# Kernel optimization log

Measured on AMD Instinct MI355X. Metric: run time of the kernel, lower is better.

## Reference

```python
import jax, jax.numpy as jnp
import numpy as np

NU, NI = 50000, 50000
N = NU + NI
NNZ = 1_000_000
DIM = 64          # dim_latent
FK = 4            # factor_k
DK = DIM // FK    # dim_k = 16
ITER_K = 2        # iterate_k
NUM_LAYER = 2     # len(dim_layer_list)
EPS = 1e-12


def setup_inputs() -> dict:
    key = jax.random.key(0)
    k1, k2, k3, k4 = jax.random.split(key, 4)
    # xavier-ish init scale for the embedding tables
    embed_user = jax.random.normal(k1, (NU, DIM), dtype=jnp.float32) * 0.1
    embed_item = jax.random.normal(k2, (NI, DIM), dtype=jnp.float32) * 0.1
    edge_head = jax.random.randint(k3, (NNZ,), 0, N, dtype=jnp.int32)
    edge_tail = jax.random.randint(k4, (NNZ,), 0, N, dtype=jnp.int32)
    return {"embed_user": embed_user, "embed_item": embed_item,
            "edge_head": edge_head, "edge_tail": edge_tail}


def _l2norm(x, axis=-1):
    # torch F.normalize(p=2): x / max(||x||, eps)
    return x / jnp.maximum(jnp.linalg.norm(x, axis=axis, keepdims=True), EPS)


def _dgcf_forward(embed_user, embed_item, head, tail):
    ego = jnp.concatenate([embed_user, embed_item], axis=0)  # [N, DIM]
    A_values = jnp.ones((FK, NNZ), dtype=ego.dtype)
    all_embed = [ego]

    def spmm(v, x):
        # sparse A (values v on edges head->tail) @ x : [N, DK]
        return jax.ops.segment_sum(v[:, None] * x[tail], head, num_segments=N)

    spmm_f = jax.vmap(spmm)  # over factor axis

    for _ in range(NUM_LAYER):
        # split ego into factor chunks: [FK, N, DK]
        xs = jnp.moveaxis(ego.reshape(N, FK, DK), 1, 0)
        factor_emb = None
        for t in range(ITER_K):
            # softmax over factors per edge; detached (as in torch .detach())
            vals = jax.lax.stop_gradient(jax.nn.softmax(A_values, axis=0))  # [FK, NNZ]
            # row sums of each factor adjacency -> D = diag(1/sqrt(rowsum))
            row_sum = jax.ops.segment_sum(vals.T, head, num_segments=N).T   # [FK, N]
            d = jnp.where(row_sum > 0,
                          1.0 / jnp.sqrt(jnp.maximum(row_sum, EPS)), 0.0)
            # factor_emb = D @ A @ D @ x  (three chained spmm in torch)
            y = spmm_f(vals, d[:, :, None] * xs)
            factor_emb = d[:, :, None] * y                                   # [FK, N, DK]
            # routing scores: sum over dim of normalize(h) * tanh(normalize(t))
            h = _l2norm(factor_emb[:, head, :], -1)                          # [FK, NNZ, DK]
            tt = _l2norm(xs[:, tail, :], -1)
            scores = jnp.sum(h * jnp.tanh(tt), axis=-1)                      # [FK, NNZ]
            A_values = A_values + scores
        # layer output: normalize last-iteration factor embeddings, re-concat
        layer_emb = _l2norm(factor_emb, -1)           # [FK, N, DK]
        ego = jnp.moveaxis(layer_emb, 0, 1).reshape(N, DIM)
        all_embed.append(ego)

    out = jnp.mean(jnp.stack(all_embed, axis=1), axis=1)  # [N, DIM]
    return out


def reference(embed_user, embed_item, edge_head, edge_tail):
    out = _dgcf_forward(embed_user, embed_item, edge_head, edge_tail)
    return out[:NU], out[NU:]
```

## Files before the change

kernel.cpp:

```cpp
#include <hip/hip_runtime.h>
#include <hip/hip_bf16.h>

#define NUSER 50000
#define NITEM 50000
#define NN    100000
#define NNZ_  1000000
#define DIM_  64
#define NBLK  391
#define EPB   2560
#define BINC  4096
#define NPAD  (NBLK * BINC)

#define FL_SVC    1
#define FL_SC     2
#define FL_NEXT   8
#define FL_FIN    16
#define FL_ACONST 32
#define FL_GN     128

static inline int ceil_div(int a, int b) { return (a + b - 1) / b; }

static __device__ inline float bf2f(unsigned short u) {
    return __uint_as_float(((unsigned int)u) << 16);
}
static __device__ inline unsigned short f2bf(float f) {
    unsigned int x = __float_as_uint(f);
    x += 0x7fffu + ((x >> 16) & 1u);
    return (unsigned short)(x >> 16);
}
static __device__ inline unsigned short f2h(float f) {
    _Float16 h = (_Float16)f;
    return __builtin_bit_cast(unsigned short, h);
}
static __device__ inline float h2f(unsigned short u) {
    return (float)__builtin_bit_cast(_Float16, u);
}

#if __has_builtin(__builtin_amdgcn_fdot2_f32_bf16)
typedef __bf16 bf16x2_t __attribute__((ext_vector_type(2)));
static __device__ inline float dot2bf(unsigned int a, unsigned int b, float c) {
    return __builtin_amdgcn_fdot2_f32_bf16(__builtin_bit_cast(bf16x2_t, a),
                                           __builtin_bit_cast(bf16x2_t, b), c, false);
}
#else
static __device__ inline float dot2bf(unsigned int a, unsigned int b, float c) {
    return c + bf2f((unsigned short)(a & 0xffffu)) * bf2f((unsigned short)(b & 0xffffu))
             + bf2f((unsigned short)(a >> 16)) * bf2f((unsigned short)(b >> 16));
}
#endif

__global__ void k_binscat(const int* __restrict__ head, const int* __restrict__ tail,
                          int* __restrict__ cursor, int* __restrict__ bin) {
    __shared__ int cnt[NBLK];
    __shared__ int chunk[NBLK];
    int tid = threadIdx.x;
    for (int i = tid; i < NBLK; i += 256) cnt[i] = 0;
    __syncthreads();
    int e0 = blockIdx.x * EPB;
    int e1 = min(e0 + EPB, NNZ_);
    for (int e = e0 + tid; e < e1; e += 256)
        atomicAdd(&cnt[head[e] >> 8], 1);
    __syncthreads();
    for (int i = tid; i < NBLK; i += 256) {
        chunk[i] = cnt[i] ? (i * BINC + atomicAdd(&cursor[i], cnt[i])) : 0;
        cnt[i] = 0;
    }
    __syncthreads();
    for (int e = e0 + tid; e < e1; e += 256) {
        int h = head[e], t = tail[e];
        int b = h >> 8;
        int off = atomicAdd(&cnt[b], 1);
        bin[chunk[b] + off] = t | ((h & 255) << 20);
    }
}

__global__ void k_bucket(const int* __restrict__ bin, const int* __restrict__ cursor,
                         int2* __restrict__ row_se, float4* __restrict__ d4a,
                         int* __restrict__ csr_tail) {
    __shared__ int deg[256];
    __shared__ int sh[256];
    __shared__ int cur[256];
    int tid = threadIdx.x;
    int b = blockIdx.x;
    int n0 = b << 8;
    int e0 = b * BINC, e1 = e0 + cursor[b];
    deg[tid] = 0;
    __syncthreads();
    for (int e = e0 + tid; e < e1; e += 256)
        atomicAdd(&deg[bin[e] >> 20], 1);
    __syncthreads();
    int myDeg = deg[tid];
    sh[tid] = myDeg;
    __syncthreads();
    for (int off = 1; off < 256; off <<= 1) {
        int u = 0;
        if (tid >= off) u = sh[tid - off];
        __syncthreads();
        sh[tid] += u;
        __syncthreads();
    }
    int loff = sh[tid] - myDeg;
    int start = b * BINC + loff;
    int n = n0 + tid;
    if (n < NN) {
        row_se[n] = make_int2(start, start + myDeg);
        float dd = (myDeg > 0) ? 2.0f / sqrtf((float)myDeg) : 0.0f;
        d4a[n] = make_float4(dd, dd, dd, dd);
    }
    cur[tid] = start;
    __syncthreads();
    for (int e = e0 + tid; e < e1; e += 256) {
        int p = bin[e];
        int pos = atomicAdd(&cur[p >> 20], 1);
        csr_tail[pos] = p & 0xFFFFF;
    }
}

__global__ void k_init(const float* __restrict__ eu, const float* __restrict__ ei,
                       const float* __restrict__ d4a,
                       unsigned short* __restrict__ ego, unsigned short* __restrict__ te,
                       unsigned short* __restrict__ G0, float* __restrict__ out) {
    int i = blockIdx.x * 256 + threadIdx.x;
    if (i >= NN * DIM_) return;
    float v = (i < NUSER * DIM_) ? eu[i] : ei[i - NUSER * DIM_];
    out[i] = v;
    ego[i] = f2bf(v);
    G0[i] = f2bf(v * d4a[i >> 4]);
    float s = v * v;
    s += __shfl_xor(s, 1); s += __shfl_xor(s, 2);
    s += __shfl_xor(s, 4); s += __shfl_xor(s, 8);
    float nrm = v / fmaxf(sqrtf(s), 1e-12f);
    float ex = __expf(2.0f * nrm);
    te[i] = f2bf((ex - 1.0f) / (ex + 1.0f));
}

template<int FLAGS, int NJ>
static __device__ __forceinline__ void iter_body(
    int n, int lane, int q, int l, int f, int r0, int r1,
    unsigned int* __restrict__ svA,
    const unsigned short* __restrict__ G,
    const unsigned short* __restrict__ te,
    const int* __restrict__ csr_tail,
    float* __restrict__ out,
    const unsigned short* __restrict__ X,
    unsigned short* __restrict__ Gn,
    unsigned short* __restrict__ egon, unsigned short* __restrict__ ten)
{
    constexpr bool needRec = !(FLAGS & FL_SVC) || ((FLAGS & FL_SC) && !(FLAGS & FL_ACONST));
    float ax = 0.f, ay = 0.f, az = 0.f, aw = 0.f;

    int ct[NJ]; float cw[NJ]; unsigned int cr[NJ]; uint2 cv[NJ];
    int eb = r0 + q;
#pragma unroll
    for (int j = 0; j < NJ; ++j) {
        int i = eb + 4 * j;
        bool v = (i < r1);
        int ic = v ? i : r0;
        int t = csr_tail[ic];
        ct[j] = v ? t : 0;
        if (needRec) cr[j] = svA[ic * 4 + f];
        float w;
        if (FLAGS & FL_SVC) w = 1.0f;
        else w = bf2f((unsigned short)(cr[j] & 0xffffu));
        cw[j] = v ? w : 0.f;
    }
#pragma unroll
    for (int j = 0; j < NJ; ++j) {
        if (FLAGS & FL_SC)
            cv[j] = *(const uint2*)(te + ct[j] * 64 + 4 * l);
    }
#pragma unroll
    for (int j = 0; j < NJ; ++j) {
        ushort4 u = *(const ushort4*)(G + ct[j] * 64 + 4 * l);
        ax += cw[j] * bf2f(u.x); ay += cw[j] * bf2f(u.y);
        az += cw[j] * bf2f(u.z); aw += cw[j] * bf2f(u.w);
    }

    if (NJ == 4) {
        for (int base = r0 + 16; base < r1; base += 16) {
            int tj[4]; float wj[4];
#pragma unroll
            for (int j = 0; j < 4; ++j) {
                int i = base + q + 4 * j;
                bool v = (i < r1);
                int ic = v ? i : r0;
                int t = csr_tail[ic];
                tj[j] = v ? t : 0;
                float w;
                if (FLAGS & FL_SVC) w = 1.0f;
                else w = bf2f((unsigned short)(svA[ic * 4 + f] & 0xffffu));
                wj[j] = v ? w : 0.f;
            }
#pragma unroll
            for (int j = 0; j < 4; ++j) {
                ushort4 u = *(const ushort4*)(G + tj[j] * 64 + 4 * l);
                ax += wj[j] * bf2f(u.x); ay += wj[j] * bf2f(u.y);
                az += wj[j] * bf2f(u.z); aw += wj[j] * bf2f(u.w);
            }
        }
    }

    ax += __shfl_xor(ax, 16); ax += __shfl_xor(ax, 32);
    ay += __shfl_xor(ay, 16); ay += __shfl_xor(ay, 32);
    az += __shfl_xor(az, 16); az += __shfl_xor(az, 32);
    aw += __shfl_xor(aw, 16); aw += __shfl_xor(aw, 32);

    float s = ax * ax + ay * ay + az * az + aw * aw;
    s += __shfl_xor(s, 1); s += __shfl_xor(s, 2);
    float inv = 1.0f / fmaxf(sqrtf(s), 1e-12f);
    float fx = ax * inv, fy = ay * inv, fz = az * inv, fw = aw * inv;

    float y = 0.f;
    if (FLAGS & (FL_NEXT | FL_FIN)) {
        int src = lane >> 2;
        float t0r = __shfl(fx, src), t1r = __shfl(fy, src);
        float t2r = __shfl(fz, src), t3r = __shfl(fw, src);
        y = (lane & 2) ? ((lane & 1) ? t3r : t2r) : ((lane & 1) ? t1r : t0r);
        int base = n * 64 + lane;
        if (FLAGS & FL_FIN) {
            out[base] = (out[base] + bf2f(X[base]) + y) * (1.0f / 3.0f);
        }
        if (FLAGS & FL_NEXT) {
            egon[base] = f2bf(y);
            float e2 = __expf(2.0f * y);
            ten[base] = f2bf((e2 - 1.0f) / (e2 + 1.0f));
        }
    }

    float accs = 0.f;
    if (FLAGS & FL_SC) {
        unsigned int p01 = ((unsigned int)f2bf(fy) << 16) | f2bf(fx);
        unsigned int p23 = ((unsigned int)f2bf(fw) << 16) | f2bf(fz);
#pragma unroll
        for (int j = 0; j < NJ; ++j) {
            int i = eb + 4 * j;
            bool v = (i < r1);
            float dot = dot2bf(cv[j].y, p23, dot2bf(cv[j].x, p01, 0.0f));
            dot += __shfl_xor(dot, 1); dot += __shfl_xor(dot, 2);
            float a = (FLAGS & FL_ACONST) ? 1.0f : h2f((unsigned short)(cr[j] >> 16));
            a += dot;
            float ex = __expf(a);
            float sum = ex;
            sum += __shfl_xor(sum, 4); sum += __shfl_xor(sum, 8);
            float sv = ex / sum;
            if (v && (l & 3) == 0)
                svA[i * 4 + f] = (unsigned int)f2bf(sv) | ((unsigned int)f2h(a) << 16);
            accs += v ? sv : 0.f;
        }
        if (NJ == 4) {
            for (int base = r0 + 16; base < r1; base += 16) {
                int tj[4]; float aj[4]; uint2 vj[4];
#pragma unroll
                for (int j = 0; j < 4; ++j) {
                    int i = base + q + 4 * j;
                    bool v = (i < r1);
                    int ic = v ? i : r0;
                    int t = csr_tail[ic];
                    tj[j] = v ? t : 0;
                    if (!(FLAGS & FL_ACONST))
                        aj[j] = h2f((unsigned short)(svA[ic * 4 + f] >> 16));
                }
#pragma unroll
                for (int j = 0; j < 4; ++j)
                    vj[j] = *(const uint2*)(te + tj[j] * 64 + 4 * l);
#pragma unroll
                for (int j = 0; j < 4; ++j) {
                    int i = base + q + 4 * j;
                    bool v = (i < r1);
                    float dot = dot2bf(vj[j].y, p23, dot2bf(vj[j].x, p01, 0.0f));
                    dot += __shfl_xor(dot, 1); dot += __shfl_xor(dot, 2);
                    float a = (FLAGS & FL_ACONST) ? 1.0f : aj[j];
                    a += dot;
                    float ex = __expf(a);
                    float sum = ex;
                    sum += __shfl_xor(sum, 4); sum += __shfl_xor(sum, 8);
                    float sv = ex / sum;
                    if (v && (l & 3) == 0)
                        svA[i * 4 + f] = (unsigned int)f2bf(sv) | ((unsigned int)f2h(a) << 16);
                    accs += v ? sv : 0.f;
                }
            }
        }
        accs += __shfl_xor(accs, 16); accs += __shfl_xor(accs, 32);
    }

    if (FLAGS & (FL_GN | FL_NEXT)) {
        float av = __shfl(accs, (lane >> 4) << 2);
        float d = (av > 0.f) ? 1.0f / sqrtf(fmaxf(av, 1e-12f)) : 0.f;
        int base = n * 64 + lane;
        float src = (FLAGS & FL_NEXT) ? y : bf2f(X[base]);
        Gn[base] = f2bf(src * d);
    }
}

template<int FLAGS>
__global__ void k_iter(unsigned int* __restrict__ svA,
                       const unsigned short* __restrict__ G,
                       const unsigned short* __restrict__ te,
                       const int2* __restrict__ row_se, const int* __restrict__ csr_tail,
                       float* __restrict__ out,
                       const unsigned short* __restrict__ X,
                       unsigned short* __restrict__ Gn,
                       unsigned short* __restrict__ egon, unsigned short* __restrict__ ten) {
    int n = (blockIdx.x * 256 + threadIdx.x) >> 6;
    if (n >= NN) return;
    int lane = threadIdx.x & 63;
    int q = lane >> 4;
    int l = lane & 15;
    int f = l >> 2;
    int2 se = row_se[n];
    int r0 = __builtin_amdgcn_readfirstlane(se.x);
    int r1 = __builtin_amdgcn_readfirstlane(se.y);
    int deg = r1 - r0;
    if (deg <= 8) {
        if (deg <= 4)
            iter_body<FLAGS, 1>(n, lane, q, l, f, r0, r1, svA, G, te,
                                csr_tail, out, X, Gn, egon, ten);
        else
            iter_body<FLAGS, 2>(n, lane, q, l, f, r0, r1, svA, G, te,
                                csr_tail, out, X, Gn, egon, ten);
    } else {
        if (deg <= 12)
            iter_body<FLAGS, 3>(n, lane, q, l, f, r0, r1, svA, G, te,
                                csr_tail, out, X, Gn, egon, ten);
        else
            iter_body<FLAGS, 4>(n, lane, q, l, f, r0, r1, svA, G, te,
                                csr_tail, out, X, Gn, egon, ten);
    }
}

extern "C" void kernel_launch(void* const* d_in, const int* in_sizes, int n_in,
                              void* d_out, int out_size, void* d_ws, size_t ws_size,
                              hipStream_t stream) {
    const float* eu = (const float*)d_in[0];
    const float* ei = (const float*)d_in[1];
    const int* head = (const int*)d_in[2];
    const int* tail = (const int*)d_in[3];
    float* out = (float*)d_out;

    unsigned int* svA = (unsigned int*)d_ws;
    float* d4a = (float*)(svA + (size_t)NPAD * 4);
    unsigned short* ego_a = (unsigned short*)(d4a + (size_t)NN * 4);
    unsigned short* te_a  = ego_a + (size_t)NN * DIM_;
    unsigned short* ego_b = te_a + (size_t)NN * DIM_;
    unsigned short* te_b  = ego_b + (size_t)NN * DIM_;
    unsigned short* Ga    = te_b + (size_t)NN * DIM_;
    unsigned short* Gb    = Ga + (size_t)NN * DIM_;
    int* csr_tail = (int*)(Gb + (size_t)NN * DIM_);
    int2* row_se = (int2*)(csr_tail + (size_t)NPAD);
    int* cursor = (int*)(row_se + NN);
    int* bin = (int*)svA;

    const int node_blocks = ceil_div(NN * DIM_, 256);
    const int wave_blocks = ceil_div(NN * 64, 256);

    hipMemsetAsync(cursor, 0, NBLK * sizeof(int), stream);
    k_binscat<<<NBLK, 256, 0, stream>>>(head, tail, cursor, bin);
    k_bucket<<<NBLK, 256, 0, stream>>>(bin, cursor, row_se, (float4*)d4a, csr_tail);

    k_init<<<node_blocks, 256, 0, stream>>>(eu, ei, d4a, ego_a, te_a, Ga, out);

    k_iter<FL_SVC | FL_SC | FL_ACONST | FL_GN><<<wave_blocks, 256, 0, stream>>>(
        svA, Ga, te_a, row_se, csr_tail, out, ego_a, Gb, ego_b, te_b);

    k_iter<FL_SC | FL_NEXT><<<wave_blocks, 256, 0, stream>>>(
        svA, Gb, te_a, row_se, csr_tail, out, ego_a, Ga, ego_b, te_b);

    k_iter<FL_SC | FL_GN><<<wave_blocks, 256, 0, stream>>>(
        svA, Ga, te_b, row_se, csr_tail, out, ego_b, Gb, ego_b, te_b);

    k_iter<FL_FIN><<<wave_blocks, 256, 0, stream>>>(
        svA, Gb, te_b, row_se, csr_tail, out, ego_b, Ga, ego_b, te_b);
}
```

Before: 335.5 us.

## Interleave factor embeddings and tanh features per node into one 256-byte row

Replaces the separate G (scaled embedding) and te (tanh of normalized embedding) buffers with one interleaved buffer per ping-pong slot. Each node row now holds 64 G values followed by 64 te values. Edge gathers by tail index therefore fetch both operands from adjacent memory, which aims to improve DRAM page and TLB locality for the random gathers. The cost is that the init kernel writes the tanh values to both slots, and the buffer roles must be tracked carefully across the four iteration kernels.

```diff
diff --git a/kernel.cpp b/kernel.cpp
--- a/kernel.cpp
+++ b/kernel.cpp
@@ -118,33 +118,36 @@
 
 __global__ void k_init(const float* __restrict__ eu, const float* __restrict__ ei,
                        const float* __restrict__ d4a,
-                       unsigned short* __restrict__ ego, unsigned short* __restrict__ te,
-                       unsigned short* __restrict__ G0, float* __restrict__ out) {
+                       unsigned short* __restrict__ ego,
+                       unsigned short* __restrict__ XTa, unsigned short* __restrict__ XTb,
+                       float* __restrict__ out) {
     int i = blockIdx.x * 256 + threadIdx.x;
     if (i >= NN * DIM_) return;
     float v = (i < NUSER * DIM_) ? eu[i] : ei[i - NUSER * DIM_];
     out[i] = v;
     ego[i] = f2bf(v);
-    G0[i] = f2bf(v * d4a[i >> 4]);
+    int xi = i + (i & ~63);
+    XTa[xi] = f2bf(v * d4a[i >> 4]);
     float s = v * v;
     s += __shfl_xor(s, 1); s += __shfl_xor(s, 2);
     s += __shfl_xor(s, 4); s += __shfl_xor(s, 8);
     float nrm = v / fmaxf(sqrtf(s), 1e-12f);
     float ex = __expf(2.0f * nrm);
-    te[i] = f2bf((ex - 1.0f) / (ex + 1.0f));
+    unsigned short tb = f2bf((ex - 1.0f) / (ex + 1.0f));
+    XTa[xi + 64] = tb;
+    XTb[xi + 64] = tb;
 }
 
 template<int FLAGS, int NJ>
 static __device__ __forceinline__ void iter_body(
     int n, int lane, int q, int l, int f, int r0, int r1,
     unsigned int* __restrict__ svA,
-    const unsigned short* __restrict__ G,
-    const unsigned short* __restrict__ te,
+    const unsigned short* __restrict__ XT,
     const int* __restrict__ csr_tail,
     float* __restrict__ out,
     const unsigned short* __restrict__ X,
-    unsigned short* __restrict__ Gn,
-    unsigned short* __restrict__ egon, unsigned short* __restrict__ ten)
+    unsigned short* __restrict__ GnXT,
+    unsigned short* __restrict__ egon)
 {
     constexpr bool needRec = !(FLAGS & FL_SVC) || ((FLAGS & FL_SC) && !(FLAGS & FL_ACONST));
     float ax = 0.f, ay = 0.f, az = 0.f, aw = 0.f;
@@ -167,11 +170,11 @@
 #pragma unroll
     for (int j = 0; j < NJ; ++j) {
         if (FLAGS & FL_SC)
-            cv[j] = *(const uint2*)(te + ct[j] * 64 + 4 * l);
+            cv[j] = *(const uint2*)(XT + ct[j] * 128 + 64 + 4 * l);
     }
 #pragma unroll
     for (int j = 0; j < NJ; ++j) {
-        ushort4 u = *(const ushort4*)(G + ct[j] * 64 + 4 * l);
+        ushort4 u = *(const ushort4*)(XT + ct[j] * 128 + 4 * l);
         ax += cw[j] * bf2f(u.x); ay += cw[j] * bf2f(u.y);
         az += cw[j] * bf2f(u.z); aw += cw[j] * bf2f(u.w);
     }
@@ -193,7 +196,7 @@
             }
 #pragma unroll
             for (int j = 0; j < 4; ++j) {
-                ushort4 u = *(const ushort4*)(G + tj[j] * 64 + 4 * l);
+                ushort4 u = *(const ushort4*)(XT + tj[j] * 128 + 4 * l);
                 ax += wj[j] * bf2f(u.x); ay += wj[j] * bf2f(u.y);
                 az += wj[j] * bf2f(u.z); aw += wj[j] * bf2f(u.w);
             }
@@ -223,7 +226,7 @@
         if (FLAGS & FL_NEXT) {
             egon[base] = f2bf(y);
             float e2 = __expf(2.0f * y);
-            ten[base] = f2bf((e2 - 1.0f) / (e2 + 1.0f));
+            GnXT[n * 128 + 64 + lane] = f2bf((e2 - 1.0f) / (e2 + 1.0f));
         }
     }
 
@@ -262,7 +265,7 @@
                 }
 #pragma unroll
                 for (int j = 0; j < 4; ++j)
-                    vj[j] = *(const uint2*)(te + tj[j] * 64 + 4 * l);
+                    vj[j] = *(const uint2*)(XT + tj[j] * 128 + 64 + 4 * l);
 #pragma unroll
                 for (int j = 0; j < 4; ++j) {
                     int i = base + q + 4 * j;
@@ -287,21 +290,19 @@
     if (FLAGS & (FL_GN | FL_NEXT)) {
         float av = __shfl(accs, (lane >> 4) << 2);
         float d = (av > 0.f) ? 1.0f / sqrtf(fmaxf(av, 1e-12f)) : 0.f;
-        int base = n * 64 + lane;
-        float src = (FLAGS & FL_NEXT) ? y : bf2f(X[base]);
-        Gn[base] = f2bf(src * d);
+        float src = (FLAGS & FL_NEXT) ? y : bf2f(X[n * 64 + lane]);
+        GnXT[n * 128 + lane] = f2bf(src * d);
     }
 }
 
 template<int FLAGS>
 __global__ void k_iter(unsigned int* __restrict__ svA,
-                       const unsigned short* __restrict__ G,
-                       const unsigned short* __restrict__ te,
+                       const unsigned short* __restrict__ XT,
                        const int2* __restrict__ row_se, const int* __restrict__ csr_tail,
                        float* __restrict__ out,
                        const unsigned short* __restrict__ X,
-                       unsigned short* __restrict__ Gn,
-                       unsigned short* __restrict__ egon, unsigned short* __restrict__ ten) {
+                       unsigned short* __restrict__ GnXT,
+                       unsigned short* __restrict__ egon) {
     int n = (blockIdx.x * 256 + threadIdx.x) >> 6;
     if (n >= NN) return;
     int lane = threadIdx.x & 63;
@@ -314,18 +315,18 @@
     int deg = r1 - r0;
     if (deg <= 8) {
         if (deg <= 4)
-            iter_body<FLAGS, 1>(n, lane, q, l, f, r0, r1, svA, G, te,
-                                csr_tail, out, X, Gn, egon, ten);
+            iter_body<FLAGS, 1>(n, lane, q, l, f, r0, r1, svA, XT,
+                                csr_tail, out, X, GnXT, egon);
         else
-            iter_body<FLAGS, 2>(n, lane, q, l, f, r0, r1, svA, G, te,
-                                csr_tail, out, X, Gn, egon, ten);
+            iter_body<FLAGS, 2>(n, lane, q, l, f, r0, r1, svA, XT,
+                                csr_tail, out, X, GnXT, egon);
     } else {
         if (deg <= 12)
-            iter_body<FLAGS, 3>(n, lane, q, l, f, r0, r1, svA, G, te,
-                                csr_tail, out, X, Gn, egon, ten);
+            iter_body<FLAGS, 3>(n, lane, q, l, f, r0, r1, svA, XT,
+                                csr_tail, out, X, GnXT, egon);
         else
-            iter_body<FLAGS, 4>(n, lane, q, l, f, r0, r1, svA, G, te,
-                                csr_tail, out, X, Gn, egon, ten);
+            iter_body<FLAGS, 4>(n, lane, q, l, f, r0, r1, svA, XT,
+                                csr_tail, out, X, GnXT, egon);
     }
 }
 
@@ -341,12 +342,10 @@
     unsigned int* svA = (unsigned int*)d_ws;
     float* d4a = (float*)(svA + (size_t)NPAD * 4);
     unsigned short* ego_a = (unsigned short*)(d4a + (size_t)NN * 4);
-    unsigned short* te_a  = ego_a + (size_t)NN * DIM_;
-    unsigned short* ego_b = te_a + (size_t)NN * DIM_;
-    unsigned short* te_b  = ego_b + (size_t)NN * DIM_;
-    unsigned short* Ga    = te_b + (size_t)NN * DIM_;
-    unsigned short* Gb    = Ga + (size_t)NN * DIM_;
-    int* csr_tail = (int*)(Gb + (size_t)NN * DIM_);
+    unsigned short* ego_b = ego_a + (size_t)NN * DIM_;
+    unsigned short* XT_A  = ego_b + (size_t)NN * DIM_;
+    unsigned short* XT_B  = XT_A + (size_t)NN * 128;
+    int* csr_tail = (int*)(XT_B + (size_t)NN * 128);
     int2* row_se = (int2*)(csr_tail + (size_t)NPAD);
     int* cursor = (int*)(row_se + NN);
     int* bin = (int*)svA;
@@ -358,17 +357,17 @@
     k_binscat<<<NBLK, 256, 0, stream>>>(head, tail, cursor, bin);
     k_bucket<<<NBLK, 256, 0, stream>>>(bin, cursor, row_se, (float4*)d4a, csr_tail);
 
-    k_init<<<node_blocks, 256, 0, stream>>>(eu, ei, d4a, ego_a, te_a, Ga, out);
+    k_init<<<node_blocks, 256, 0, stream>>>(eu, ei, d4a, ego_a, XT_A, XT_B, out);
 
     k_iter<FL_SVC | FL_SC | FL_ACONST | FL_GN><<<wave_blocks, 256, 0, stream>>>(
-        svA, Ga, te_a, row_se, csr_tail, out, ego_a, Gb, ego_b, te_b);
+        svA, XT_A, row_se, csr_tail, out, ego_a, XT_B, ego_b);
 
     k_iter<FL_SC | FL_NEXT><<<wave_blocks, 256, 0, stream>>>(
-        svA, Gb, te_a, row_se, csr_tail, out, ego_a, Ga, ego_b, te_b);
+        svA, XT_B, row_se, csr_tail, out, ego_a, XT_A, ego_b);
 
     k_iter<FL_SC | FL_GN><<<wave_blocks, 256, 0, stream>>>(
-        svA, Ga, te_b, row_se, csr_tail, out, ego_b, Gb, ego_b, te_b);
+        svA, XT_A, row_se, csr_tail, out, ego_b, XT_B, ego_b);
 
     k_iter<FL_FIN><<<wave_blocks, 256, 0, stream>>>(
-        svA, Gb, te_b, row_se, csr_tail, out, ego_b, Ga, ego_b, te_b);
-}
+        svA, XT_B, row_se, csr_tail, out, ego_b, XT_A, ego_b);
+}
```

Result: no change. 340.3 us (+1.4%).

## Remap wave lanes to 8 edges x 8 dims with 16-byte gathers

Applied to the files above, without the earlier changes.

Changes the per-node wave mapping from 4 edges by 16 lanes of 4 bf16 to 8 edges by 8 lanes of 8 bf16. Gathers of G and tanh embeddings become 16-byte loads, and each lane handles more dims per edge. Reductions, the softmax shuffles, the output index mapping and the degree dispatch (now two variants) are reworked to match. The aim is fewer, wider memory transactions and more edges in flight per wave. In exchange each lane holds more registers and cross-lane reductions gain an extra step.

```diff
diff --git a/kernel.cpp b/kernel.cpp
--- a/kernel.cpp
+++ b/kernel.cpp
@@ -23,6 +23,12 @@
 static __device__ inline float bf2f(unsigned short u) {
     return __uint_as_float(((unsigned int)u) << 16);
 }
+static __device__ inline float blo(unsigned int u) {
+    return __uint_as_float(u << 16);
+}
+static __device__ inline float bhi(unsigned int u) {
+    return __uint_as_float(u & 0xffff0000u);
+}
 static __device__ inline unsigned short f2bf(float f) {
     unsigned int x = __float_as_uint(f);
     x += 0x7fffu + ((x >> 16) & 1u);
@@ -44,8 +50,7 @@
 }
 #else
 static __device__ inline float dot2bf(unsigned int a, unsigned int b, float c) {
-    return c + bf2f((unsigned short)(a & 0xffffu)) * bf2f((unsigned short)(b & 0xffffu))
-             + bf2f((unsigned short)(a >> 16)) * bf2f((unsigned short)(b >> 16));
+    return c + blo(a) * blo(b) + bhi(a) * bhi(b);
 }
 #endif
 
@@ -134,9 +139,11 @@
     te[i] = f2bf((ex - 1.0f) / (ex + 1.0f));
 }
 
+#define QRED(a) { a += __shfl_xor(a, 8); a += __shfl_xor(a, 16); a += __shfl_xor(a, 32); }
+
 template<int FLAGS, int NJ>
 static __device__ __forceinline__ void iter_body(
-    int n, int lane, int q, int l, int f, int r0, int r1,
+    int n, int lane, int q, int l8, int f2, int r0, int r1,
     unsigned int* __restrict__ svA,
     const unsigned short* __restrict__ G,
     const unsigned short* __restrict__ te,
@@ -147,18 +154,19 @@
     unsigned short* __restrict__ egon, unsigned short* __restrict__ ten)
 {
     constexpr bool needRec = !(FLAGS & FL_SVC) || ((FLAGS & FL_SC) && !(FLAGS & FL_ACONST));
-    float ax = 0.f, ay = 0.f, az = 0.f, aw = 0.f;
-
-    int ct[NJ]; float cw[NJ]; unsigned int cr[NJ]; uint2 cv[NJ];
-    int eb = r0 + q;
+    int deg = r1 - r0;
+    float a0 = 0.f, a1 = 0.f, a2 = 0.f, a3 = 0.f;
+    float a4 = 0.f, a5 = 0.f, a6 = 0.f, a7 = 0.f;
+
+    int ct[NJ]; float cw[NJ]; unsigned int cr[NJ]; uint4 cv[NJ];
 #pragma unroll
     for (int j = 0; j < NJ; ++j) {
-        int i = eb + 4 * j;
+        int i = r0 + q + 8 * j;
         bool v = (i < r1);
         int ic = v ? i : r0;
         int t = csr_tail[ic];
         ct[j] = v ? t : 0;
-        if (needRec) cr[j] = svA[ic * 4 + f];
+        if (needRec) cr[j] = svA[ic * 4 + f2];
         float w;
         if (FLAGS & FL_SVC) w = 1.0f;
         else w = bf2f((unsigned short)(cr[j] & 0xffffu));
@@ -167,56 +175,53 @@
 #pragma unroll
     for (int j = 0; j < NJ; ++j) {
         if (FLAGS & FL_SC)
-            cv[j] = *(const uint2*)(te + ct[j] * 64 + 4 * l);
+            cv[j] = *(const uint4*)(te + ct[j] * 64 + 8 * l8);
     }
 #pragma unroll
     for (int j = 0; j < NJ; ++j) {
-        ushort4 u = *(const ushort4*)(G + ct[j] * 64 + 4 * l);
-        ax += cw[j] * bf2f(u.x); ay += cw[j] * bf2f(u.y);
-        az += cw[j] * bf2f(u.z); aw += cw[j] * bf2f(u.w);
-    }
-
-    if (NJ == 4) {
-        for (int base = r0 + 16; base < r1; base += 16) {
-            int tj[4]; float wj[4];
-#pragma unroll
-            for (int j = 0; j < 4; ++j) {
-                int i = base + q + 4 * j;
-                bool v = (i < r1);
-                int ic = v ? i : r0;
-                int t = csr_tail[ic];
-                tj[j] = v ? t : 0;
-                float w;
-                if (FLAGS & FL_SVC) w = 1.0f;
-                else w = bf2f((unsigned short)(svA[ic * 4 + f] & 0xffffu));
-                wj[j] = v ? w : 0.f;
-            }
-#pragma unroll
-            for (int j = 0; j < 4; ++j) {
-                ushort4 u = *(const ushort4*)(G + tj[j] * 64 + 4 * l);
-                ax += wj[j] * bf2f(u.x); ay += wj[j] * bf2f(u.y);
-                az += wj[j] * bf2f(u.z); aw += wj[j] * bf2f(u.w);
-            }
-        }
-    }
-
-    ax += __shfl_xor(ax, 16); ax += __shfl_xor(ax, 32);
-    ay += __shfl_xor(ay, 16); ay += __shfl_xor(ay, 32);
-    az += __shfl_xor(az, 16); az += __shfl_xor(az, 32);
-    aw += __shfl_xor(aw, 16); aw += __shfl_xor(aw, 32);
-
-    float s = ax * ax + ay * ay + az * az + aw * aw;
-    s += __shfl_xor(s, 1); s += __shfl_xor(s, 2);
+        uint4 gu = *(const uint4*)(G + ct[j] * 64 + 8 * l8);
+        float w = cw[j];
+        a0 += w * blo(gu.x); a1 += w * bhi(gu.x);
+        a2 += w * blo(gu.y); a3 += w * bhi(gu.y);
+        a4 += w * blo(gu.z); a5 += w * bhi(gu.z);
+        a6 += w * blo(gu.w); a7 += w * bhi(gu.w);
+    }
+
+    if (NJ == 2) {
+        for (int base = r0 + 16; base < r1; base += 8) {
+            int i = base + q;
+            bool v = (i < r1);
+            int ic = v ? i : r0;
+            int t = csr_tail[ic];
+            t = v ? t : 0;
+            float w;
+            if (FLAGS & FL_SVC) w = 1.0f;
+            else w = bf2f((unsigned short)(svA[ic * 4 + f2] & 0xffffu));
+            w = v ? w : 0.f;
+            uint4 gu = *(const uint4*)(G + t * 64 + 8 * l8);
+            a0 += w * blo(gu.x); a1 += w * bhi(gu.x);
+            a2 += w * blo(gu.y); a3 += w * bhi(gu.y);
+            a4 += w * blo(gu.z); a5 += w * bhi(gu.z);
+            a6 += w * blo(gu.w); a7 += w * bhi(gu.w);
+        }
+    }
+
+    QRED(a0) QRED(a1) QRED(a2) QRED(a3)
+    QRED(a4) QRED(a5) QRED(a6) QRED(a7)
+
+    float s = a0 * a0 + a1 * a1 + a2 * a2 + a3 * a3
+            + a4 * a4 + a5 * a5 + a6 * a6 + a7 * a7;
+    s += __shfl_xor(s, 1);
     float inv = 1.0f / fmaxf(sqrtf(s), 1e-12f);
-    float fx = ax * inv, fy = ay * inv, fz = az * inv, fw = aw * inv;
-
+    float f0 = a0 * inv, f1 = a1 * inv, f2v = a2 * inv, f3 = a3 * inv;
+    float f4 = a4 * inv, f5 = a5 * inv, f6 = a6 * inv, f7 = a7 * inv;
+
+    int k = 8 * l8 + q;
     float y = 0.f;
     if (FLAGS & (FL_NEXT | FL_FIN)) {
-        int src = lane >> 2;
-        float t0r = __shfl(fx, src), t1r = __shfl(fy, src);
-        float t2r = __shfl(fz, src), t3r = __shfl(fw, src);
-        y = (lane & 2) ? ((lane & 1) ? t3r : t2r) : ((lane & 1) ? t1r : t0r);
-        int base = n * 64 + lane;
+        y = (q & 4) ? ((q & 2) ? ((q & 1) ? f7 : f6) : ((q & 1) ? f5 : f4))
+                    : ((q & 2) ? ((q & 1) ? f3 : f2v) : ((q & 1) ? f1 : f0));
+        int base = n * 64 + k;
         if (FLAGS & FL_FIN) {
             out[base] = (out[base] + bf2f(X[base]) + y) * (1.0f / 3.0f);
         }
@@ -229,65 +234,59 @@
 
     float accs = 0.f;
     if (FLAGS & FL_SC) {
-        unsigned int p01 = ((unsigned int)f2bf(fy) << 16) | f2bf(fx);
-        unsigned int p23 = ((unsigned int)f2bf(fw) << 16) | f2bf(fz);
+        unsigned int p0 = ((unsigned int)f2bf(f1) << 16) | f2bf(f0);
+        unsigned int p1 = ((unsigned int)f2bf(f3) << 16) | f2bf(f2v);
+        unsigned int p2 = ((unsigned int)f2bf(f5) << 16) | f2bf(f4);
+        unsigned int p3 = ((unsigned int)f2bf(f7) << 16) | f2bf(f6);
 #pragma unroll
         for (int j = 0; j < NJ; ++j) {
-            int i = eb + 4 * j;
+            int i = r0 + q + 8 * j;
             bool v = (i < r1);
-            float dot = dot2bf(cv[j].y, p23, dot2bf(cv[j].x, p01, 0.0f));
-            dot += __shfl_xor(dot, 1); dot += __shfl_xor(dot, 2);
+            float dot = dot2bf(cv[j].w, p3, dot2bf(cv[j].z, p2,
+                        dot2bf(cv[j].y, p1, dot2bf(cv[j].x, p0, 0.0f))));
+            dot += __shfl_xor(dot, 1);
             float a = (FLAGS & FL_ACONST) ? 1.0f : h2f((unsigned short)(cr[j] >> 16));
             a += dot;
             float ex = __expf(a);
             float sum = ex;
-            sum += __shfl_xor(sum, 4); sum += __shfl_xor(sum, 8);
+            sum += __shfl_xor(sum, 2); sum += __shfl_xor(sum, 4);
             float sv = ex / sum;
-            if (v && (l & 3) == 0)
-                svA[i * 4 + f] = (unsigned int)f2bf(sv) | ((unsigned int)f2h(a) << 16);
+            if (v && (l8 & 1) == 0)
+                svA[i * 4 + f2] = (unsigned int)f2bf(sv) | ((unsigned int)f2h(a) << 16);
             accs += v ? sv : 0.f;
         }
-        if (NJ == 4) {
-            for (int base = r0 + 16; base < r1; base += 16) {
-                int tj[4]; float aj[4]; uint2 vj[4];
-#pragma unroll
-                for (int j = 0; j < 4; ++j) {
-                    int i = base + q + 4 * j;
-                    bool v = (i < r1);
-                    int ic = v ? i : r0;
-                    int t = csr_tail[ic];
-                    tj[j] = v ? t : 0;
-                    if (!(FLAGS & FL_ACONST))
-                        aj[j] = h2f((unsigned short)(svA[ic * 4 + f] >> 16));
-                }
-#pragma unroll
-                for (int j = 0; j < 4; ++j)
-                    vj[j] = *(const uint2*)(te + tj[j] * 64 + 4 * l);
-#pragma unroll
-                for (int j = 0; j < 4; ++j) {
-                    int i = base + q + 4 * j;
-                    bool v = (i < r1);
-                    float dot = dot2bf(vj[j].y, p23, dot2bf(vj[j].x, p01, 0.0f));
-                    dot += __shfl_xor(dot, 1); dot += __shfl_xor(dot, 2);
-                    float a = (FLAGS & FL_ACONST) ? 1.0f : aj[j];
-                    a += dot;
-                    float ex = __expf(a);
-                    float sum = ex;
-                    sum += __shfl_xor(sum, 4); sum += __shfl_xor(sum, 8);
-                    float sv = ex / sum;
-                    if (v && (l & 3) == 0)
-                        svA[i * 4 + f] = (unsigned int)f2bf(sv) | ((unsigned int)f2h(a) << 16);
-                    accs += v ? sv : 0.f;
-                }
+        if (NJ == 2) {
+            for (int base = r0 + 16; base < r1; base += 8) {
+                int i = base + q;
+                bool v = (i < r1);
+                int ic = v ? i : r0;
+                int t = csr_tail[ic];
+                t = v ? t : 0;
+                float aj = 1.0f;
+                if (!(FLAGS & FL_ACONST))
+                    aj = h2f((unsigned short)(svA[ic * 4 + f2] >> 16));
+                uint4 tv = *(const uint4*)(te + t * 64 + 8 * l8);
+                float dot = dot2bf(tv.w, p3, dot2bf(tv.z, p2,
+                            dot2bf(tv.y, p1, dot2bf(tv.x, p0, 0.0f))));
+                dot += __shfl_xor(dot, 1);
+                float a = aj + dot;
+                float ex = __expf(a);
+                float sum = ex;
+                sum += __shfl_xor(sum, 2); sum += __shfl_xor(sum, 4);
+                float sv = ex / sum;
+                if (v && (l8 & 1) == 0)
+                    svA[i * 4 + f2] = (unsigned int)f2bf(sv) | ((unsigned int)f2h(a) << 16);
+                accs += v ? sv : 0.f;
             }
         }
-        accs += __shfl_xor(accs, 16); accs += __shfl_xor(accs, 32);
+        QRED(accs)
     }
 
     if (FLAGS & (FL_GN | FL_NEXT)) {
-        float av = __shfl(accs, (lane >> 4) << 2);
+        int fo = k >> 4;
+        float av = __shfl(accs, 2 * fo);
         float d = (av > 0.f) ? 1.0f / sqrtf(fmaxf(av, 1e-12f)) : 0.f;
-        int base = n * 64 + lane;
+        int base = n * 64 + k;
         float src = (FLAGS & FL_NEXT) ? y : bf2f(X[base]);
         Gn[base] = f2bf(src * d);
     }
@@ -305,28 +304,18 @@
     int n = (blockIdx.x * 256 + threadIdx.x) >> 6;
     if (n >= NN) return;
     int lane = threadIdx.x & 63;
-    int q = lane >> 4;
-    int l = lane & 15;
-    int f = l >> 2;
+    int q = lane >> 3;
+    int l8 = lane & 7;
+    int f2 = l8 >> 1;
     int2 se = row_se[n];
     int r0 = __builtin_amdgcn_readfirstlane(se.x);
     int r1 = __builtin_amdgcn_readfirstlane(se.y);
-    int deg = r1 - r0;
-    if (deg <= 8) {
-        if (deg <= 4)
-            iter_body<FLAGS, 1>(n, lane, q, l, f, r0, r1, svA, G, te,
-                                csr_tail, out, X, Gn, egon, ten);
-        else
-            iter_body<FLAGS, 2>(n, lane, q, l, f, r0, r1, svA, G, te,
-                                csr_tail, out, X, Gn, egon, ten);
-    } else {
-        if (deg <= 12)
-            iter_body<FLAGS, 3>(n, lane, q, l, f, r0, r1, svA, G, te,
-                                csr_tail, out, X, Gn, egon, ten);
-        else
-            iter_body<FLAGS, 4>(n, lane, q, l, f, r0, r1, svA, G, te,
-                                csr_tail, out, X, Gn, egon, ten);
-    }
+    if (r1 - r0 <= 8)
+        iter_body<FLAGS, 1>(n, lane, q, l8, f2, r0, r1, svA, G, te,
+                            csr_tail, out, X, Gn, egon, ten);
+    else
+        iter_body<FLAGS, 2>(n, lane, q, l8, f2, r0, r1, svA, G, te,
+                            csr_tail, out, X, Gn, egon, ten);
 }
 
 extern "C" void kernel_launch(void* const* d_in, const int* in_sizes, int n_in,
```

Measured after the change: 322.1 us. 4.0% less time.
